# Optimization experiments

Measured on AMD Instinct MI355X. Metric: run time of the kernel, lower is better.

The kernel has to match this reference:

```python
import jax, jax.numpy as jnp
import numpy as np

B, H, KVH, D, X = 16, 16, 4, 128, 4      # batch, q heads, kv heads, head dim, fp32 cache packing (X=16//elem_size)
BLK, MAXB = 16, 256                       # vllm block size, max kv blocks per seq (max_seqlen=4096)
NB = B * MAXB                             # total physical kv-cache blocks
MAX_NNZ = 64                              # max attended kv blocks per (head, query-block) row
LOCAL, STRIDE = 32, 8                     # local window (in vllm blocks) and vertical stride


def _build_layout():
    # Per-head CSR over vllm-block granularity: block kb attended by query block m iff
    # it is in the causal local window or on the head's stride phase.
    crow = np.zeros((H, MAXB + 1), np.int32)
    cols_per_head = []
    for h in range(H):
        cols = []
        for m in range(MAXB):
            ks = [kb for kb in range(m + 1) if (m - kb) < LOCAL or kb % STRIDE == h % STRIDE]
            ks = ks[-MAX_NNZ:]
            crow[h, m + 1] = crow[h, m] + len(ks)
            cols.extend(ks)
        cols_per_head.append(cols)
    maxlen = max(len(c) for c in cols_per_head)
    col = np.zeros((H, maxlen), np.int32)
    for h, c in enumerate(cols_per_head):
        col[h, :len(c)] = np.asarray(c, np.int32)
    return jnp.asarray(crow), jnp.asarray(col)


def setup_inputs() -> dict:
    key = jax.random.key(0)
    k1, k2, k3, k4 = jax.random.split(key, 4)
    q = jax.random.normal(k1, (B, H, D), dtype=jnp.float32)
    # vLLM paged caches: K [NB, KVH, D//X, BLK, X], V [NB, KVH, D, BLK]
    k_cache = jax.random.normal(k2, (NB, KVH, D // X, BLK, X), dtype=jnp.float32)
    v_cache = jax.random.normal(k3, (NB, KVH, D, BLK), dtype=jnp.float32)
    block_tables = jnp.arange(NB, dtype=jnp.int32).reshape(B, MAXB)
    context_lens = jax.random.randint(k4, (B,), 64, MAXB * BLK + 1).astype(jnp.int32)
    layout_crow, layout_col = _build_layout()
    return {"q": q, "k_cache": k_cache, "v_cache": v_cache,
            "block_tables": block_tables, "context_lens": context_lens,
            "layout_crow": layout_crow, "layout_col": layout_col}


def reference(q, k_cache, v_cache, block_tables, context_lens, layout_crow, layout_col):
    sm_scale = 1.0 / float(np.sqrt(D))
    q_pid = context_lens.astype(jnp.int32) - 1             # [B] decode-token position
    pbid = q_pid // BLK                                     # [B] query block row in CSR layout
    h_idx = jnp.arange(H)
    hkv = h_idx // (H // KVH)                               # kv head for each q head
    start = layout_crow[h_idx[None, :], pbid[:, None]]      # [B,H]
    end = layout_crow[h_idx[None, :], pbid[:, None] + 1]    # [B,H]
    j = jnp.arange(MAX_NNZ)
    idx = start[:, :, None] + j                             # [B,H,J]
    valid = idx < end[:, :, None]
    idx = jnp.clip(idx, 0, layout_col.shape[1] - 1)
    cols = layout_col[h_idx[None, :, None], idx]            # [B,H,J] logical kv block ids
    bt = block_tables[jnp.arange(B)[:, None, None], cols]   # [B,H,J] physical cache block ids
    # K block load mirrors the Triton pointer math: [D//X, BLK, X] -> [D//X, X, BLK] -> [D, BLK]
    kb = k_cache[bt, hkv[None, :, None]]                    # [B,H,J,D//X,BLK,X]
    kb = jnp.transpose(kb, (0, 1, 2, 3, 5, 4)).reshape(B, H, MAX_NNZ, D, BLK)
    vb = v_cache[bt, hkv[None, :, None]]                    # [B,H,J,D,BLK]
    scores = jnp.einsum('bhd,bhjdn->bhjn', q, kb) * sm_scale
    pos = cols[..., None] * BLK + jnp.arange(BLK)           # [B,H,J,BLK] absolute token positions
    mask = valid[..., None] & (pos <= q_pid[:, None, None, None])  # causal + block-validity
    scores = jnp.where(mask, scores, -jnp.inf)
    p = jax.nn.softmax(scores.reshape(B, H, -1), axis=-1).reshape(B, H, MAX_NNZ, BLK)
    out = jnp.einsum('bhjn,bhjdn->bhd', p, vb)              # [B,H,D]
    return out
```

## Files before the change

kernel.cpp:

```cpp
#include <hip/hip_runtime.h>
#include <math.h>

constexpr int B = 16, H = 16, KVH = 4, D = 128;
constexpr int BLK = 16, MAXB = 256, MAX_NNZ = 64;
constexpr int GRP = H / KVH;
constexpr int NSPLIT = 4;
constexpr int JPS = MAX_NNZ / NSPLIT;

constexpr int WSTRIDE = D + 2;

__global__ __launch_bounds__(256) void sparse_attn_split(
    const float* __restrict__ q,
    const float* __restrict__ k_cache,
    const float* __restrict__ v_cache,
    const int* __restrict__ block_tables,
    const int* __restrict__ context_lens,
    const int* __restrict__ layout_crow,
    const int* __restrict__ layout_col,
    int collen,
    float* __restrict__ ws)
{
    const int bh = blockIdx.x >> 2;
    const int split = blockIdx.x & (NSPLIT - 1);
    const int b = bh / H;
    const int h = bh % H;
    const int hkv = h / GRP;
    const int tid = threadIdx.x;
    const int lane = tid & 63;
    const int wv = tid >> 6;

    const int q_pid = context_lens[b] - 1;
    const int pbid = q_pid / BLK;
    const int row_off = h * (MAXB + 1) + pbid;
    const int start = layout_crow[row_off];
    const int nnz = layout_crow[row_off + 1] - start;
    const int j0 = split * JPS;
    const int jcnt = min(JPS, nnz - j0);

    __shared__ float s_q[D];
    __shared__ float s_p[JPS * BLK];
    __shared__ int   s_bt[JPS];
    __shared__ int   s_col[JPS];
    __shared__ float s_red[4];

    if (tid < D) s_q[tid] = q[(b * H + h) * D + tid];
    if (tid < JPS) {
        int c = 0;
        if (tid < jcnt) c = layout_col[h * collen + start + j0 + tid];
        s_col[tid] = c;
        s_bt[tid] = block_tables[b * MAXB + c];
    }
    __syncthreads();

    const float sm_scale = 0.08838834764831845f;

    const int j = tid >> 4;
    const int n = tid & 15;
    float sc = -INFINITY;
    if (j < jcnt) {
        const int pos = s_col[j] * BLK + n;
        if (pos <= q_pid) {
            const float4* kb = (const float4*)(k_cache + (size_t)(s_bt[j] * KVH + hkv) * (D * BLK));
            const float4* qv4 = (const float4*)s_q;
            float acc = 0.f;
            #pragma unroll
            for (int d1 = 0; d1 < 32; ++d1) {
                const float4 kv = kb[d1 * 16 + n];
                const float4 qv = qv4[d1];
                acc += kv.x * qv.x + kv.y * qv.y + kv.z * qv.z + kv.w * qv.w;
            }
            sc = acc * sm_scale;
        }
    }

    float m = sc;
    #pragma unroll
    for (int off = 1; off < 64; off <<= 1)
        m = fmaxf(m, __shfl_xor(m, off));
    if (lane == 0) s_red[wv] = m;
    __syncthreads();
    m = fmaxf(fmaxf(s_red[0], s_red[1]), fmaxf(s_red[2], s_red[3]));

    const float p = (sc == -INFINITY) ? 0.f : __expf(sc - m);
    s_p[tid] = p;
    float s = p;
    #pragma unroll
    for (int off = 1; off < 64; off <<= 1)
        s += __shfl_xor(s, off);
    __syncthreads();
    if (lane == 0) s_red[wv] = s;
    __syncthreads();
    const float ssum = s_red[0] + s_red[1] + s_red[2] + s_red[3];

    float acc = 0.f;
    for (int jj = 0; jj < jcnt; ++jj) {
        const float4* vb = (const float4*)(v_cache + (size_t)(s_bt[jj] * KVH + hkv) * (D * BLK));
        const float4 v0 = vb[tid * 2];
        const float4 v1 = vb[tid * 2 + 1];
        const float4 p0 = ((const float4*)s_p)[jj * 4 + (tid & 1) * 2];
        const float4 p1 = ((const float4*)s_p)[jj * 4 + (tid & 1) * 2 + 1];
        acc += v0.x * p0.x + v0.y * p0.y + v0.z * p0.z + v0.w * p0.w
             + v1.x * p1.x + v1.y * p1.y + v1.z * p1.z + v1.w * p1.w;
    }
    acc += __shfl_xor(acc, 1);

    float* wsp = ws + (size_t)(bh * NSPLIT + split) * WSTRIDE;
    if ((tid & 1) == 0) wsp[tid >> 1] = acc;
    if (tid == 0) { wsp[D] = m; wsp[D + 1] = ssum; }
}

__global__ __launch_bounds__(128) void sparse_attn_combine(
    const float* __restrict__ ws,
    float* __restrict__ out)
{
    const int bh = blockIdx.x;
    const int d = threadIdx.x;
    const float* base = ws + (size_t)bh * NSPLIT * WSTRIDE;

    float m = -INFINITY;
    #pragma unroll
    for (int sidx = 0; sidx < NSPLIT; ++sidx)
        m = fmaxf(m, base[sidx * WSTRIDE + D]);

    float num = 0.f, den = 0.f;
    #pragma unroll
    for (int sidx = 0; sidx < NSPLIT; ++sidx) {
        const float ms = base[sidx * WSTRIDE + D];
        const float ss = base[sidx * WSTRIDE + D + 1];
        const float a = (ms == -INFINITY) ? 0.f : __expf(ms - m);
        num += base[sidx * WSTRIDE + d] * a;
        den += ss * a;
    }
    out[bh * D + d] = num / den;
}

extern "C" void kernel_launch(void* const* d_in, const int* in_sizes, int n_in,
                              void* d_out, int out_size, void* d_ws, size_t ws_size,
                              hipStream_t stream) {
    const float* q            = (const float*)d_in[0];
    const float* k_cache      = (const float*)d_in[1];
    const float* v_cache      = (const float*)d_in[2];
    const int*   block_tables = (const int*)d_in[3];
    const int*   context_lens = (const int*)d_in[4];
    const int*   layout_crow  = (const int*)d_in[5];
    const int*   layout_col   = (const int*)d_in[6];
    const int    collen       = in_sizes[6] / H;
    float* out = (float*)d_out;
    float* ws  = (float*)d_ws;

    sparse_attn_split<<<B * H * NSPLIT, 256, 0, stream>>>(
        q, k_cache, v_cache, block_tables, context_lens,
        layout_crow, layout_col, collen, ws);
    sparse_attn_combine<<<B * H, 128, 0, stream>>>(ws, out);
}
```

Measured before the change: 30.60 us.

## Share KV block loads across GQA head group via per-group union of sparse columns

Adds a kernel that builds, for each (batch, kv-head) group, the union of the sparse kv-block columns attended by its four query heads, each entry tagged with a per-head bitmask. The attention kernel then loads each K/V block once and computes scores and PV for all four query heads, masking out heads that do not attend that block. The work is split into 16 slices per group, and the combine kernel merges 16 partials per head. The aim is to cut redundant K/V global traffic across heads that share a kv head, at the cost of an extra launch, more registers and LDS per block, and a larger combine step.

```diff
diff --git a/kernel.cpp b/kernel.cpp
--- a/kernel.cpp
+++ b/kernel.cpp
@@ -4,50 +4,103 @@
 constexpr int B = 16, H = 16, KVH = 4, D = 128;
 constexpr int BLK = 16, MAXB = 256, MAX_NNZ = 64;
 constexpr int GRP = H / KVH;
-constexpr int NSPLIT = 4;
-constexpr int JPS = MAX_NNZ / NSPLIT;
-
+constexpr int NSL = 16;
+constexpr int UENT = 1 + 256;
+constexpr int PART_OFF = 16640;
 constexpr int WSTRIDE = D + 2;
 
-__global__ __launch_bounds__(256) void sparse_attn_split(
+__global__ __launch_bounds__(256) void build_union(
+    const int* __restrict__ context_lens,
+    const int* __restrict__ layout_crow,
+    const int* __restrict__ layout_col,
+    int collen,
+    int* __restrict__ wsA)
+{
+    const int gidx = blockIdx.x;
+    const int b = gidx >> 2, hkv = gidx & 3;
+    const int tid = threadIdx.x;
+    const int g = tid >> 6, lane = tid & 63;
+
+    __shared__ unsigned s_bm[GRP][8];
+    if (tid < 32) s_bm[tid >> 3][tid & 7] = 0u;
+    __syncthreads();
+
+    const int q_pid = context_lens[b] - 1;
+    const int pbid = q_pid / BLK;
+    const int h_abs = hkv * GRP + g;
+    const int start = layout_crow[h_abs * (MAXB + 1) + pbid];
+    const int end   = layout_crow[h_abs * (MAXB + 1) + pbid + 1];
+    if (start + lane < end) {
+        const int c = layout_col[h_abs * collen + start + lane];
+        atomicOr(&s_bm[g][c >> 5], 1u << (c & 31));
+    }
+    __syncthreads();
+
+    if (tid < 8) {
+        unsigned un[8]; int pre = 0, total = 0;
+        #pragma unroll
+        for (int w = 0; w < 8; ++w) {
+            const unsigned u = s_bm[0][w] | s_bm[1][w] | s_bm[2][w] | s_bm[3][w];
+            un[w] = u;
+            if (w < tid) pre += __popc(u);
+            total += __popc(u);
+        }
+        int* base = wsA + gidx * UENT;
+        if (tid == 0) base[0] = total;
+        unsigned u = un[tid];
+        int k = pre;
+        while (u) {
+            const int bit = __ffs(u) - 1; u &= u - 1;
+            const int c = tid * 32 + bit;
+            const int mask = ((s_bm[0][tid] >> bit) & 1)
+                           | (((s_bm[1][tid] >> bit) & 1) << 1)
+                           | (((s_bm[2][tid] >> bit) & 1) << 2)
+                           | (((s_bm[3][tid] >> bit) & 1) << 3);
+            base[1 + k++] = c | (mask << 16);
+        }
+    }
+}
+
+__global__ __launch_bounds__(256) void sparse_attn_slice(
     const float* __restrict__ q,
     const float* __restrict__ k_cache,
     const float* __restrict__ v_cache,
     const int* __restrict__ block_tables,
     const int* __restrict__ context_lens,
-    const int* __restrict__ layout_crow,
-    const int* __restrict__ layout_col,
-    int collen,
-    float* __restrict__ ws)
+    const int* __restrict__ wsA,
+    float* __restrict__ wsB)
 {
-    const int bh = blockIdx.x >> 2;
-    const int split = blockIdx.x & (NSPLIT - 1);
-    const int b = bh / H;
-    const int h = bh % H;
-    const int hkv = h / GRP;
+    const int wg = blockIdx.x;
+    const int gidx = wg >> 4;
+    const int slice = wg & (NSL - 1);
+    const int b = gidx >> 2, hkv = gidx & 3;
     const int tid = threadIdx.x;
     const int lane = tid & 63;
     const int wv = tid >> 6;
 
     const int q_pid = context_lens[b] - 1;
-    const int pbid = q_pid / BLK;
-    const int row_off = h * (MAXB + 1) + pbid;
-    const int start = layout_crow[row_off];
-    const int nnz = layout_crow[row_off + 1] - start;
-    const int j0 = split * JPS;
-    const int jcnt = min(JPS, nnz - j0);
-
-    __shared__ float s_q[D];
-    __shared__ float s_p[JPS * BLK];
-    __shared__ int   s_bt[JPS];
-    __shared__ int   s_col[JPS];
-    __shared__ float s_red[4];
-
-    if (tid < D) s_q[tid] = q[(b * H + h) * D + tid];
-    if (tid < JPS) {
-        int c = 0;
-        if (tid < jcnt) c = layout_col[h * collen + start + j0 + tid];
-        s_col[tid] = c;
+    const int U = wsA[gidx * UENT];
+    const int L = (U + NSL - 1) / NSL;
+    const int lo = slice * L;
+    const int cnt = min(U, lo + L) - lo;
+
+    __shared__ float s_q[GRP * D];
+    __shared__ float s_p[GRP][256];
+    __shared__ int   s_col[16];
+    __shared__ int   s_msk[16];
+    __shared__ int   s_bt[16];
+    __shared__ float s_redm[GRP][4];
+    __shared__ float s_reds[GRP][4];
+
+    for (int i = tid; i < GRP * D; i += 256)
+        s_q[i] = q[(b * H + hkv * GRP + (i >> 7)) * D + (i & 127)];
+    if (tid < 16) {
+        int c = 0, mk = 0;
+        if (tid < cnt) {
+            const int e = wsA[gidx * UENT + 1 + lo + tid];
+            c = e & 0xFFFF; mk = e >> 16;
+        }
+        s_col[tid] = c; s_msk[tid] = mk;
         s_bt[tid] = block_tables[b * MAXB + c];
     }
     __syncthreads();
@@ -56,79 +109,123 @@
 
     const int j = tid >> 4;
     const int n = tid & 15;
-    float sc = -INFINITY;
-    if (j < jcnt) {
+    float sc[GRP];
+    #pragma unroll
+    for (int h = 0; h < GRP; ++h) sc[h] = -INFINITY;
+    if (j < cnt) {
         const int pos = s_col[j] * BLK + n;
         if (pos <= q_pid) {
             const float4* kb = (const float4*)(k_cache + (size_t)(s_bt[j] * KVH + hkv) * (D * BLK));
             const float4* qv4 = (const float4*)s_q;
-            float acc = 0.f;
+            float acc[GRP] = {0.f, 0.f, 0.f, 0.f};
             #pragma unroll
             for (int d1 = 0; d1 < 32; ++d1) {
                 const float4 kv = kb[d1 * 16 + n];
-                const float4 qv = qv4[d1];
-                acc += kv.x * qv.x + kv.y * qv.y + kv.z * qv.z + kv.w * qv.w;
+                #pragma unroll
+                for (int h = 0; h < GRP; ++h) {
+                    const float4 qv = qv4[h * 32 + d1];
+                    acc[h] += kv.x * qv.x + kv.y * qv.y + kv.z * qv.z + kv.w * qv.w;
+                }
             }
-            sc = acc * sm_scale;
-        }
-    }
-
-    float m = sc;
-    #pragma unroll
-    for (int off = 1; off < 64; off <<= 1)
-        m = fmaxf(m, __shfl_xor(m, off));
-    if (lane == 0) s_red[wv] = m;
-    __syncthreads();
-    m = fmaxf(fmaxf(s_red[0], s_red[1]), fmaxf(s_red[2], s_red[3]));
-
-    const float p = (sc == -INFINITY) ? 0.f : __expf(sc - m);
-    s_p[tid] = p;
-    float s = p;
-    #pragma unroll
-    for (int off = 1; off < 64; off <<= 1)
-        s += __shfl_xor(s, off);
-    __syncthreads();
-    if (lane == 0) s_red[wv] = s;
-    __syncthreads();
-    const float ssum = s_red[0] + s_red[1] + s_red[2] + s_red[3];
-
-    float acc = 0.f;
-    for (int jj = 0; jj < jcnt; ++jj) {
+            const int mk = s_msk[j];
+            #pragma unroll
+            for (int h = 0; h < GRP; ++h)
+                if ((mk >> h) & 1) sc[h] = acc[h] * sm_scale;
+        }
+    }
+
+    float m[GRP];
+    #pragma unroll
+    for (int h = 0; h < GRP; ++h) {
+        float v = sc[h];
+        #pragma unroll
+        for (int off = 1; off < 64; off <<= 1)
+            v = fmaxf(v, __shfl_xor(v, off));
+        m[h] = v;
+    }
+    if (lane == 0) {
+        #pragma unroll
+        for (int h = 0; h < GRP; ++h) s_redm[h][wv] = m[h];
+    }
+    __syncthreads();
+    float ssum[GRP];
+    #pragma unroll
+    for (int h = 0; h < GRP; ++h) {
+        m[h] = fmaxf(fmaxf(s_redm[h][0], s_redm[h][1]), fmaxf(s_redm[h][2], s_redm[h][3]));
+        const float p = (sc[h] == -INFINITY) ? 0.f : __expf(sc[h] - m[h]);
+        s_p[h][tid] = p;
+        float v = p;
+        #pragma unroll
+        for (int off = 1; off < 64; off <<= 1)
+            v += __shfl_xor(v, off);
+        ssum[h] = v;
+    }
+    if (lane == 0) {
+        #pragma unroll
+        for (int h = 0; h < GRP; ++h) s_reds[h][wv] = ssum[h];
+    }
+    __syncthreads();
+    #pragma unroll
+    for (int h = 0; h < GRP; ++h)
+        ssum[h] = s_reds[h][0] + s_reds[h][1] + s_reds[h][2] + s_reds[h][3];
+
+    float acc[GRP] = {0.f, 0.f, 0.f, 0.f};
+    for (int jj = 0; jj < cnt; ++jj) {
         const float4* vb = (const float4*)(v_cache + (size_t)(s_bt[jj] * KVH + hkv) * (D * BLK));
         const float4 v0 = vb[tid * 2];
         const float4 v1 = vb[tid * 2 + 1];
-        const float4 p0 = ((const float4*)s_p)[jj * 4 + (tid & 1) * 2];
-        const float4 p1 = ((const float4*)s_p)[jj * 4 + (tid & 1) * 2 + 1];
-        acc += v0.x * p0.x + v0.y * p0.y + v0.z * p0.z + v0.w * p0.w
-             + v1.x * p1.x + v1.y * p1.y + v1.z * p1.z + v1.w * p1.w;
-    }
-    acc += __shfl_xor(acc, 1);
-
-    float* wsp = ws + (size_t)(bh * NSPLIT + split) * WSTRIDE;
-    if ((tid & 1) == 0) wsp[tid >> 1] = acc;
-    if (tid == 0) { wsp[D] = m; wsp[D + 1] = ssum; }
+        const int pbase = jj * 4 + (tid & 1) * 2;
+        #pragma unroll
+        for (int h = 0; h < GRP; ++h) {
+            const float4 p0 = ((const float4*)s_p[h])[pbase];
+            const float4 p1 = ((const float4*)s_p[h])[pbase + 1];
+            acc[h] += v0.x * p0.x + v0.y * p0.y + v0.z * p0.z + v0.w * p0.w
+                    + v1.x * p1.x + v1.y * p1.y + v1.z * p1.z + v1.w * p1.w;
+        }
+    }
+    #pragma unroll
+    for (int h = 0; h < GRP; ++h)
+        acc[h] += __shfl_xor(acc[h], 1);
+
+    float* pb = wsB + (size_t)((gidx * NSL + slice) * GRP) * WSTRIDE;
+    if ((tid & 1) == 0) {
+        #pragma unroll
+        for (int h = 0; h < GRP; ++h)
+            pb[h * WSTRIDE + (tid >> 1)] = acc[h];
+    }
+    if (tid == 0) {
+        #pragma unroll
+        for (int h = 0; h < GRP; ++h) {
+            pb[h * WSTRIDE + D] = m[h];
+            pb[h * WSTRIDE + D + 1] = ssum[h];
+        }
+    }
 }
 
 __global__ __launch_bounds__(128) void sparse_attn_combine(
-    const float* __restrict__ ws,
+    const float* __restrict__ wsB,
     float* __restrict__ out)
 {
     const int bh = blockIdx.x;
+    const int h = bh & (H - 1);
+    const int gidx = (bh >> 4) * 4 + (h >> 2);
+    const int g = h & 3;
     const int d = threadIdx.x;
-    const float* base = ws + (size_t)bh * NSPLIT * WSTRIDE;
+
+    const float* base = wsB + (size_t)(gidx * NSL * GRP + g) * WSTRIDE;
 
     float m = -INFINITY;
     #pragma unroll
-    for (int sidx = 0; sidx < NSPLIT; ++sidx)
-        m = fmaxf(m, base[sidx * WSTRIDE + D]);
+    for (int s = 0; s < NSL; ++s)
+        m = fmaxf(m, base[s * GRP * WSTRIDE + D]);
 
     float num = 0.f, den = 0.f;
     #pragma unroll
-    for (int sidx = 0; sidx < NSPLIT; ++sidx) {
-        const float ms = base[sidx * WSTRIDE + D];
-        const float ss = base[sidx * WSTRIDE + D + 1];
+    for (int s = 0; s < NSL; ++s) {
+        const float ms = base[s * GRP * WSTRIDE + D];
+        const float ss = base[s * GRP * WSTRIDE + D + 1];
         const float a = (ms == -INFINITY) ? 0.f : __expf(ms - m);
-        num += base[sidx * WSTRIDE + d] * a;
+        num += base[s * GRP * WSTRIDE + d] * a;
         den += ss * a;
     }
     out[bh * D + d] = num / den;
@@ -146,10 +243,11 @@
     const int*   layout_col   = (const int*)d_in[6];
     const int    collen       = in_sizes[6] / H;
     float* out = (float*)d_out;
-    float* ws  = (float*)d_ws;
-
-    sparse_attn_split<<<B * H * NSPLIT, 256, 0, stream>>>(
-        q, k_cache, v_cache, block_tables, context_lens,
-        layout_crow, layout_col, collen, ws);
-    sparse_attn_combine<<<B * H, 128, 0, stream>>>(ws, out);
-}
+    int*   wsA = (int*)d_ws;
+    float* wsB = (float*)d_ws + PART_OFF;
+
+    build_union<<<B * KVH, 256, 0, stream>>>(context_lens, layout_crow, layout_col, collen, wsA);
+    sparse_attn_slice<<<B * KVH * NSL, 256, 0, stream>>>(
+        q, k_cache, v_cache, block_tables, context_lens, wsA, wsB);
+    sparse_attn_combine<<<B * H, 128, 0, stream>>>(wsB, out);
+}
```

Result: slower. 33.87 us (+10.7%).

## Split KV blocks 16-way with 64-thread per-block QK dot and early exit

Applied to the files above, without the earlier changes.

Raises the number of splits per (batch, head) from 4 to 16, so each workgroup handles 4 KV blocks instead of 16. The QK dot product for each KV block is now spread over 64 threads: each thread covers a quarter of the head dimension, and partials are combined with lane shuffles. Splits that fall beyond the row's nonzero count exit early after writing neutral workspace entries. One barrier is removed and an occupancy hint is added to launch bounds. The aim is more parallelism and shorter dependency chains in a memory-latency-bound decode kernel, at the cost of more workgroups, more workspace traffic and a longer combine loop.

```diff
diff --git a/kernel.cpp b/kernel.cpp
--- a/kernel.cpp
+++ b/kernel.cpp
@@ -3,13 +3,11 @@
 
 constexpr int B = 16, H = 16, KVH = 4, D = 128;
 constexpr int BLK = 16, MAXB = 256, MAX_NNZ = 64;
-constexpr int GRP = H / KVH;
-constexpr int NSPLIT = 4;
+constexpr int NSPLIT = 16;
 constexpr int JPS = MAX_NNZ / NSPLIT;
-
 constexpr int WSTRIDE = D + 2;
 
-__global__ __launch_bounds__(256) void sparse_attn_split(
+__global__ __launch_bounds__(256, 6) void sparse_attn_split(
     const float* __restrict__ q,
     const float* __restrict__ k_cache,
     const float* __restrict__ v_cache,
@@ -20,33 +18,41 @@
     int collen,
     float* __restrict__ ws)
 {
-    const int bh = blockIdx.x >> 2;
-    const int split = blockIdx.x & (NSPLIT - 1);
-    const int b = bh / H;
-    const int h = bh % H;
-    const int hkv = h / GRP;
+    const int bid = blockIdx.x;
+    const int bh = bid >> 4;
+    const int split = bid & (NSPLIT - 1);
+    const int b = bh >> 4;
+    const int h = bh & (H - 1);
+    const int hkv = h >> 2;
     const int tid = threadIdx.x;
-    const int lane = tid & 63;
-    const int wv = tid >> 6;
 
     const int q_pid = context_lens[b] - 1;
-    const int pbid = q_pid / BLK;
-    const int row_off = h * (MAXB + 1) + pbid;
-    const int start = layout_crow[row_off];
-    const int nnz = layout_crow[row_off + 1] - start;
+    const int pbid = q_pid >> 4;
+    const int row = h * (MAXB + 1) + pbid;
+    const int start = layout_crow[row];
+    const int nnz = layout_crow[row + 1] - start;
     const int j0 = split * JPS;
-    const int jcnt = min(JPS, nnz - j0);
+    const int cnt = min(JPS, nnz - j0);
+
+    float* wsp = ws + (size_t)(bh * NSPLIT + split) * WSTRIDE;
+    if (cnt <= 0) {
+        if (tid < D) wsp[tid] = 0.f;
+        else if (tid == D) wsp[D] = -INFINITY;
+        else if (tid == D + 1) wsp[D + 1] = 0.f;
+        return;
+    }
 
     __shared__ float s_q[D];
     __shared__ float s_p[JPS * BLK];
     __shared__ int   s_bt[JPS];
     __shared__ int   s_col[JPS];
-    __shared__ float s_red[4];
+    __shared__ float s_redm[4];
+    __shared__ float s_reds[4];
 
-    if (tid < D) s_q[tid] = q[(b * H + h) * D + tid];
+    if (tid < D) s_q[tid] = q[bh * D + tid];
     if (tid < JPS) {
         int c = 0;
-        if (tid < jcnt) c = layout_col[h * collen + start + j0 + tid];
+        if (tid < cnt) c = layout_col[h * collen + start + j0 + tid];
         s_col[tid] = c;
         s_bt[tid] = block_tables[b * MAXB + c];
     }
@@ -54,58 +60,61 @@
 
     const float sm_scale = 0.08838834764831845f;
 
-    const int j = tid >> 4;
-    const int n = tid & 15;
+    const int jw = tid >> 6;
+    const int n  = (tid >> 2) & 15;
+    const int dq = tid & 3;
     float sc = -INFINITY;
-    if (j < jcnt) {
-        const int pos = s_col[j] * BLK + n;
+    if (jw < cnt) {
+        const int pos = s_col[jw] * BLK + n;
         if (pos <= q_pid) {
-            const float4* kb = (const float4*)(k_cache + (size_t)(s_bt[j] * KVH + hkv) * (D * BLK));
-            const float4* qv4 = (const float4*)s_q;
+            const float4* kb = (const float4*)(k_cache + (size_t)(s_bt[jw] * KVH + hkv) * (D * BLK));
+            const float4* q4 = (const float4*)s_q;
             float acc = 0.f;
             #pragma unroll
-            for (int d1 = 0; d1 < 32; ++d1) {
+            for (int i = 0; i < 8; ++i) {
+                const int d1 = dq * 8 + i;
                 const float4 kv = kb[d1 * 16 + n];
-                const float4 qv = qv4[d1];
+                const float4 qv = q4[d1];
                 acc += kv.x * qv.x + kv.y * qv.y + kv.z * qv.z + kv.w * qv.w;
             }
+            acc += __shfl_xor(acc, 1);
+            acc += __shfl_xor(acc, 2);
             sc = acc * sm_scale;
         }
     }
 
     float m = sc;
     #pragma unroll
-    for (int off = 1; off < 64; off <<= 1)
+    for (int off = 4; off < 64; off <<= 1)
         m = fmaxf(m, __shfl_xor(m, off));
-    if (lane == 0) s_red[wv] = m;
+    if ((tid & 63) == 0) s_redm[jw] = m;
     __syncthreads();
-    m = fmaxf(fmaxf(s_red[0], s_red[1]), fmaxf(s_red[2], s_red[3]));
+    m = fmaxf(fmaxf(s_redm[0], s_redm[1]), fmaxf(s_redm[2], s_redm[3]));
 
-    const float p = (sc == -INFINITY) ? 0.f : __expf(sc - m);
-    s_p[tid] = p;
-    float s = p;
+    const float p = __expf(sc - m);
+    float ps = p;
     #pragma unroll
-    for (int off = 1; off < 64; off <<= 1)
-        s += __shfl_xor(s, off);
+    for (int off = 4; off < 64; off <<= 1)
+        ps += __shfl_xor(ps, off);
+    if (dq == 0) s_p[jw * BLK + n] = p;
+    if ((tid & 63) == 0) s_reds[jw] = ps;
     __syncthreads();
-    if (lane == 0) s_red[wv] = s;
-    __syncthreads();
-    const float ssum = s_red[0] + s_red[1] + s_red[2] + s_red[3];
+    const float ssum = s_reds[0] + s_reds[1] + s_reds[2] + s_reds[3];
 
+    const int dh = tid & 1;
     float acc = 0.f;
-    for (int jj = 0; jj < jcnt; ++jj) {
+    for (int jj = 0; jj < cnt; ++jj) {
         const float4* vb = (const float4*)(v_cache + (size_t)(s_bt[jj] * KVH + hkv) * (D * BLK));
         const float4 v0 = vb[tid * 2];
         const float4 v1 = vb[tid * 2 + 1];
-        const float4 p0 = ((const float4*)s_p)[jj * 4 + (tid & 1) * 2];
-        const float4 p1 = ((const float4*)s_p)[jj * 4 + (tid & 1) * 2 + 1];
+        const float4* p4 = (const float4*)(s_p + jj * BLK);
+        const float4 p0 = p4[dh * 2];
+        const float4 p1 = p4[dh * 2 + 1];
         acc += v0.x * p0.x + v0.y * p0.y + v0.z * p0.z + v0.w * p0.w
              + v1.x * p1.x + v1.y * p1.y + v1.z * p1.z + v1.w * p1.w;
     }
     acc += __shfl_xor(acc, 1);
-
-    float* wsp = ws + (size_t)(bh * NSPLIT + split) * WSTRIDE;
-    if ((tid & 1) == 0) wsp[tid >> 1] = acc;
+    if (dh == 0) wsp[tid >> 1] = acc;
     if (tid == 0) { wsp[D] = m; wsp[D + 1] = ssum; }
 }
 
@@ -119,16 +128,16 @@
 
     float m = -INFINITY;
     #pragma unroll
-    for (int sidx = 0; sidx < NSPLIT; ++sidx)
-        m = fmaxf(m, base[sidx * WSTRIDE + D]);
+    for (int s = 0; s < NSPLIT; ++s)
+        m = fmaxf(m, base[s * WSTRIDE + D]);
 
     float num = 0.f, den = 0.f;
     #pragma unroll
-    for (int sidx = 0; sidx < NSPLIT; ++sidx) {
-        const float ms = base[sidx * WSTRIDE + D];
-        const float ss = base[sidx * WSTRIDE + D + 1];
+    for (int s = 0; s < NSPLIT; ++s) {
+        const float ms = base[s * WSTRIDE + D];
+        const float ss = base[s * WSTRIDE + D + 1];
         const float a = (ms == -INFINITY) ? 0.f : __expf(ms - m);
-        num += base[sidx * WSTRIDE + d] * a;
+        num += base[s * WSTRIDE + d] * a;
         den += ss * a;
     }
     out[bh * D + d] = num / den;
```

Result: slower. 32.91 us (+7.5%).
